# Optimization experiments

Hardware: AMD Instinct MI355X
Metric: run time of the kernel (lower is better)

Reference implementation:

```python
import jax, jax.numpy as jnp
import numpy as np


def setup_inputs() -> dict:
    key = jax.random.key(0)
    ks = jax.random.split(key, 10)
    N, E = 50000, 1600000
    IN, H, OUT = 32, 64, 16
    x = jax.random.normal(ks[0], (N, IN), dtype=jnp.float32)
    edge_index = jax.random.randint(ks[1], (2, E), 0, N, dtype=jnp.int64)
    edge_attr = jax.random.normal(ks[2], (E, 3), dtype=jnp.float32)
    s1 = 1.0 / np.sqrt(2 * IN + 3)
    W1 = jax.random.uniform(ks[3], (2 * IN + 3, H), jnp.float32, -s1, s1)
    b1 = jax.random.uniform(ks[4], (H,), jnp.float32, -s1, s1)
    s2 = 1.0 / np.sqrt(H)
    W2 = jax.random.uniform(ks[5], (H, H), jnp.float32, -s2, s2)
    b2 = jax.random.uniform(ks[6], (H,), jnp.float32, -s2, s2)
    Wo = jax.random.uniform(ks[7], (H, OUT), jnp.float32, -s2, s2)
    bo = jax.random.uniform(ks[8], (OUT,), jnp.float32, -s2, s2)
    return {"x": x, "edge_index": edge_index, "edge_attr": edge_attr,
            "W1": W1, "b1": b1, "W2": W2, "b2": b2, "Wo": Wo, "bo": bo}


def reference(x, edge_index, edge_attr, W1, b1, W2, b2, Wo, bo):
    N = x.shape[0]
    src, dst = edge_index[0], edge_index[1]  # PyG: x_j = x[src], x_i = x[dst]
    x_i = x[dst]                      # [E, IN]
    x_j = x[src]                      # [E, IN]
    tmp = jnp.concatenate([x_i, x_j - x_i, edge_attr], axis=1)  # [E, 2*IN+3]
    h = jax.nn.relu(tmp @ W1 + b1)    # [E, H]
    msg = h @ W2 + b2                 # [E, H]
    # max-aggregate messages to destination nodes; empty segments -> 0 (PyG fill)
    agg = jax.ops.segment_max(msg, dst, num_segments=N)
    agg = jnp.where(jnp.isfinite(agg), agg, 0.0)
    out = jax.nn.sigmoid(agg @ Wo + bo)  # [N, OUT]
    return out
```

## Files before the change

kernel.cpp:

```cpp
#include <hip/hip_runtime.h>

#define IN_F 32
#define HID 64
#define OUTF 16
#define NSUB 8
#define SB_CAP 16
#define OVF_CAP 65536
#define ORD_NEG_INF 0x007FFFFFu

typedef _Float16 v8h __attribute__((ext_vector_type(8)));
typedef float v4f __attribute__((ext_vector_type(4)));

__device__ __forceinline__ unsigned ordenc(float v) {
  unsigned b = __float_as_uint(v);
  return (b & 0x80000000u) ? ~b : (b | 0x80000000u);
}
__device__ __forceinline__ float orddec(unsigned u) {
  unsigned b = (u & 0x80000000u) ? (u & 0x7FFFFFFFu) : ~u;
  return __uint_as_float(b);
}
__device__ __forceinline__ unsigned short f2h_bits(float f) {
  _Float16 h = (_Float16)f; unsigned short u; __builtin_memcpy(&u, &h, 2); return u;
}
__device__ __forceinline__ float h_bits2f(unsigned short u) {
  _Float16 h; __builtin_memcpy(&h, &u, 2); return (float)h;
}

__global__ __launch_bounds__(256) void pre_scatter_kernel(
    const float* __restrict__ x, const int* __restrict__ ei,
    const float* __restrict__ ea, const float* __restrict__ W1,
    const float* __restrict__ b1,
    float* __restrict__ P, float* __restrict__ Q,
    uint2* __restrict__ rec, int* __restrict__ cnt,
    int* __restrict__ ovf, int* __restrict__ ovf_cnt,
    int E, int N, int nSB)
{
  if (blockIdx.x < (unsigned)nSB) {
    const int t = threadIdx.x;
    const int base = blockIdx.x * 1024;
    const int g = blockIdx.x & (NSUB - 1);
    int e[4], s[4], d[4], pos[4];
    bool v[4];
#pragma unroll
    for (int i = 0; i < 4; ++i) {
      e[i] = base + i * 256 + t;
      v[i] = e[i] < E;
      int ec = v[i] ? e[i] : 0;
      s[i] = ei[ec];
      d[i] = ei[(size_t)E + ec];
    }
#pragma unroll
    for (int i = 0; i < 4; ++i)
      pos[i] = v[i] ? atomicAdd(&cnt[d[i] * NSUB + g], 1) : SB_CAP;
    float a0[4], a1[4], a2[4];
#pragma unroll
    for (int i = 0; i < 4; ++i) {
      int ec = v[i] ? e[i] : 0;
      a0[i] = ea[ec * 3 + 0]; a1[i] = ea[ec * 3 + 1]; a2[i] = ea[ec * 3 + 2];
    }
#pragma unroll
    for (int i = 0; i < 4; ++i) {
      if (!v[i]) continue;
      if (pos[i] < SB_CAP) {
        uint2 r;
        r.x = (unsigned)s[i] | ((unsigned)f2h_bits(a0[i]) << 16);
        r.y = (unsigned)f2h_bits(a1[i]) | ((unsigned)f2h_bits(a2[i]) << 16);
        rec[((size_t)d[i] * NSUB + g) * SB_CAP + pos[i]] = r;
      } else {
        int oi = atomicAdd(ovf_cnt, 1);
        if (oi < OVF_CAP) ovf[oi] = e[i];
      }
    }
    return;
  }
  const int lane = threadIdx.x & 63;
  float w1d[IN_F], w1b[IN_F];
#pragma unroll
  for (int c = 0; c < IN_F; ++c) {
    w1b[c] = W1[(IN_F + c) * HID + lane];
    w1d[c] = W1[c * HID + lane] - w1b[c];
  }
  const float b1v = b1[lane];
  int gw = __builtin_amdgcn_readfirstlane((((int)blockIdx.x - nSB) << 2) | (threadIdx.x >> 6));
  const int nwaves = 512 << 2;
  for (int n = gw; n < N; n += nwaves) {
    float p = b1v, q = 0.f;
#pragma unroll
    for (int c = 0; c < IN_F; ++c) {
      float xv = x[n * IN_F + c];
      p = fmaf(xv, w1d[c], p);
      q = fmaf(xv, w1b[c], q);
    }
    P[n * HID + lane] = p;
    Q[n * HID + lane] = q;
  }
}

__global__ __launch_bounds__(256) void bucket_kernel(
    const uint2* __restrict__ rec, const int* __restrict__ cnt,
    const float* __restrict__ W1, const float* __restrict__ W2,
    const float* __restrict__ P, const float* __restrict__ Q,
    unsigned* __restrict__ agg, int N)
{
  __shared__ __align__(16) _Float16 hB[4][16][72];

  const int wave = threadIdx.x >> 6;
  const int lane = threadIdx.x & 63;
  const int quad = lane >> 4;
  const int eidx = lane & 15;
  const int mych = ((eidx >> 2) << 4) + (quad << 2) + (eidx & 3);

  v8h a_frag[4][2];
#pragma unroll
  for (int t = 0; t < 4; ++t)
#pragma unroll
    for (int ks = 0; ks < 2; ++ks)
#pragma unroll
      for (int j = 0; j < 8; ++j)
        a_frag[t][ks][j] = (_Float16)W2[(ks * 32 + quad * 8 + j) * HID + t * 16 + eidx];

  const float w1c0 = W1[(2 * IN_F + 0) * HID + lane];
  const float w1c1 = W1[(2 * IN_F + 1) * HID + lane];
  const float w1c2 = W1[(2 * IN_F + 2) * HID + lane];

  const int gwave = __builtin_amdgcn_readfirstlane((blockIdx.x << 2) | wave);
  const int nw = gridDim.x << 2;

  int d = gwave;
  if (d >= N) return;

  int m; uint2 r0, r1; float pP;
  auto prefetch = [&](int dd) {
    const uint4 ca = *(const uint4*)&cnt[(size_t)dd * NSUB];
    const uint4 cb = *(const uint4*)&cnt[(size_t)dd * NSUB + 4];
    int c0 = min((int)ca.x, SB_CAP), c1 = min((int)ca.y, SB_CAP);
    int c2 = min((int)ca.z, SB_CAP), c3 = min((int)ca.w, SB_CAP);
    int c4 = min((int)cb.x, SB_CAP), c5 = min((int)cb.y, SB_CAP);
    int c6 = min((int)cb.z, SB_CAP), c7 = min((int)cb.w, SB_CAP);
    int p1 = c0, p2 = p1 + c1, p3 = p2 + c2, p4 = p3 + c3;
    int p5 = p4 + c4, p6 = p5 + c5, p7 = p6 + c6;
    m = p7 + c7;
#pragma unroll
    for (int rr = 0; rr < 2; ++rr) {
      int i = rr * 64 + lane;
      if (i < m) {
        int g = 0, base = 0;
        if (i >= p1) { g = 1; base = p1; }
        if (i >= p2) { g = 2; base = p2; }
        if (i >= p3) { g = 3; base = p3; }
        if (i >= p4) { g = 4; base = p4; }
        if (i >= p5) { g = 5; base = p5; }
        if (i >= p6) { g = 6; base = p6; }
        if (i >= p7) { g = 7; base = p7; }
        uint2 rv = rec[((size_t)dd * NSUB + g) * SB_CAP + (i - base)];
        if (rr == 0) r0 = rv; else r1 = rv;
      }
    }
    pP = P[(size_t)dd * HID + lane];
  };

  prefetch(d);

  while (d < N) {
    const int dn = d + nw;
    const int m_cur = m;
    const float pvl = pP;
    uint2 ra = r0, rb = r1;

    if (m_cur > 0) {
      {
        const int lm = m_cur - 1;
        unsigned rlx, rly;
        if (lm < 64) {
          rlx = (unsigned)__builtin_amdgcn_readlane((int)ra.x, lm);
          rly = (unsigned)__builtin_amdgcn_readlane((int)ra.y, lm);
        } else {
          rlx = (unsigned)__builtin_amdgcn_readlane((int)rb.x, lm & 63);
          rly = (unsigned)__builtin_amdgcn_readlane((int)rb.y, lm & 63);
        }
        if (lane >= m_cur)      { ra.x = rlx; ra.y = rly; }
        if (lane + 64 >= m_cur) { rb.x = rlx; rb.y = rly; }
      }

      float qv[16];
#pragma unroll
      for (int i = 0; i < 16; ++i) {
        unsigned sx = (unsigned)__builtin_amdgcn_readlane((int)ra.x, i) & 0xFFFFu;
        qv[i] = Q[(size_t)sx * HID + lane];
      }

      if (dn < N) prefetch(dn);

      float maxv[4][4];
#pragma unroll
      for (int t = 0; t < 4; ++t)
#pragma unroll
        for (int r = 0; r < 4; ++r) maxv[t][r] = -INFINITY;

      const int ntile = (m_cur + 15) >> 4;
      for (int tb = 0; tb < ntile; ++tb) {
        uint2 rs;
        rs.x = (tb < 4) ? ra.x : rb.x;
        rs.y = (tb < 4) ? ra.y : rb.y;
        const int b16 = (tb & 3) << 4;
#pragma unroll
        for (int i = 0; i < 16; ++i) {
          const unsigned rx = (unsigned)__builtin_amdgcn_readlane((int)rs.x, b16 + i);
          const unsigned ry = (unsigned)__builtin_amdgcn_readlane((int)rs.y, b16 + i);
          float pre = pvl + qv[i];
          pre = fmaf(h_bits2f((unsigned short)(rx >> 16)), w1c0, pre);
          pre = fmaf(h_bits2f((unsigned short)(ry & 0xFFFFu)), w1c1, pre);
          pre = fmaf(h_bits2f((unsigned short)(ry >> 16)), w1c2, pre);
          hB[wave][i][lane] = (_Float16)fmaxf(pre, 0.f);
        }
        if (tb + 1 < ntile) {
          const unsigned rnx = (tb + 1 < 4) ? ra.x : rb.x;
          const int b16n = ((tb + 1) & 3) << 4;
#pragma unroll
          for (int i = 0; i < 16; ++i) {
            unsigned sx = (unsigned)__builtin_amdgcn_readlane((int)rnx, b16n + i) & 0xFFFFu;
            qv[i] = Q[(size_t)sx * HID + lane];
          }
        }
        __builtin_amdgcn_wave_barrier();

        const v8h bf0 = *(const v8h*)&hB[wave][eidx][quad * 8];
        const v8h bf1 = *(const v8h*)&hB[wave][eidx][32 + quad * 8];
#pragma unroll
        for (int t = 0; t < 4; ++t) {
          v4f acc = (v4f){0.f, 0.f, 0.f, 0.f};
          acc = __builtin_amdgcn_mfma_f32_16x16x32_f16(a_frag[t][0], bf0, acc, 0, 0, 0);
          acc = __builtin_amdgcn_mfma_f32_16x16x32_f16(a_frag[t][1], bf1, acc, 0, 0, 0);
#pragma unroll
          for (int r = 0; r < 4; ++r) maxv[t][r] = fmaxf(maxv[t][r], acc[r]);
        }
        __builtin_amdgcn_wave_barrier();
      }

#pragma unroll
      for (int t = 0; t < 4; ++t)
#pragma unroll
        for (int r = 0; r < 4; ++r) {
          float v = maxv[t][r];
          v = fmaxf(v, __shfl_xor(v, 1, 64));
          v = fmaxf(v, __shfl_xor(v, 2, 64));
          v = fmaxf(v, __shfl_xor(v, 4, 64));
          v = fmaxf(v, __shfl_xor(v, 8, 64));
          maxv[t][r] = v;
        }
      float val = maxv[0][0];
#pragma unroll
      for (int t = 0; t < 4; ++t)
#pragma unroll
        for (int r = 0; r < 4; ++r)
          val = (eidx == t * 4 + r) ? maxv[t][r] : val;
      agg[(size_t)d * HID + mych] = ordenc(val);
    } else {
      if (dn < N) prefetch(dn);
      agg[(size_t)d * HID + lane] = ORD_NEG_INF;
    }
    d = dn;
  }
}

__global__ __launch_bounds__(256) void overflow_kernel(
    const int* __restrict__ ei, const float* __restrict__ ea,
    const float* __restrict__ W1, const float* __restrict__ W2,
    const float* __restrict__ P, const float* __restrict__ Q,
    const int* __restrict__ ovf, const int* __restrict__ ovf_cnt,
    unsigned* __restrict__ agg, int E)
{
  __shared__ float hsh[4][HID];
  const int wave = threadIdx.x >> 6;
  const int lane = threadIdx.x & 63;

  int M = *ovf_cnt;
  if (M > OVF_CAP) M = OVF_CAP;
  if (M == 0) return;

  float w2r[HID];
#pragma unroll
  for (int j = 0; j < HID; ++j) w2r[j] = W2[j * HID + lane];
  const float w1c0 = W1[(2 * IN_F + 0) * HID + lane];
  const float w1c1 = W1[(2 * IN_F + 1) * HID + lane];
  const float w1c2 = W1[(2 * IN_F + 2) * HID + lane];

  const int gwave = __builtin_amdgcn_readfirstlane((blockIdx.x << 2) | wave);
  const int nw = gridDim.x << 2;
  for (int k = gwave; k < M; k += nw) {
    int e = ovf[k];
    int s = ei[e];
    int d = ei[(size_t)E + e];
    float pre = P[(size_t)d * HID + lane] + Q[(size_t)s * HID + lane];
    pre = fmaf(ea[e * 3 + 0], w1c0, pre);
    pre = fmaf(ea[e * 3 + 1], w1c1, pre);
    pre = fmaf(ea[e * 3 + 2], w1c2, pre);
    hsh[wave][lane] = fmaxf(pre, 0.f);
    __builtin_amdgcn_wave_barrier();
    float mv = 0.f;
#pragma unroll
    for (int j = 0; j < HID; ++j) mv = fmaf(hsh[wave][j], w2r[j], mv);
    atomicMax(&agg[(size_t)d * HID + lane], ordenc(mv));
    __builtin_amdgcn_wave_barrier();
  }
}

__global__ __launch_bounds__(256) void out_kernel(
    const unsigned* __restrict__ agg,
    const float* __restrict__ b2,
    const float* __restrict__ Wo, const float* __restrict__ bo,
    float* __restrict__ out, int N)
{
  __shared__ float Wos[HID * OUTF];
  __shared__ float bos[OUTF];
  __shared__ float b2s[HID];
  __shared__ float aggs[16][HID + 1];

  for (int i = threadIdx.x; i < HID * OUTF; i += 256) Wos[i] = Wo[i];
  if (threadIdx.x < OUTF) bos[threadIdx.x] = bo[threadIdx.x];
  if (threadIdx.x < HID) b2s[threadIdx.x] = b2[threadIdx.x];
  __syncthreads();

  const int nodeBase = blockIdx.x * 16;
  {
    int ln = threadIdx.x >> 4;
    int k0 = (threadIdx.x & 15) * 4;
    int n = nodeBase + ln;
    if (n < N) {
      const uint4 u = *(const uint4*)&agg[n * HID + k0];
      aggs[ln][k0 + 0] = (u.x == ORD_NEG_INF) ? 0.f : orddec(u.x) + b2s[k0 + 0];
      aggs[ln][k0 + 1] = (u.y == ORD_NEG_INF) ? 0.f : orddec(u.y) + b2s[k0 + 1];
      aggs[ln][k0 + 2] = (u.z == ORD_NEG_INF) ? 0.f : orddec(u.z) + b2s[k0 + 2];
      aggs[ln][k0 + 3] = (u.w == ORD_NEG_INF) ? 0.f : orddec(u.w) + b2s[k0 + 3];
    }
  }
  __syncthreads();
  {
    int ln = threadIdx.x >> 4;
    int o = threadIdx.x & 15;
    int n = nodeBase + ln;
    if (n < N) {
      float acc = bos[o];
#pragma unroll
      for (int k = 0; k < HID; ++k) acc = fmaf(aggs[ln][k], Wos[k * OUTF + o], acc);
      out[n * OUTF + o] = 1.f / (1.f + __expf(-acc));
    }
  }
}

extern "C" void kernel_launch(void* const* d_in, const int* in_sizes, int n_in,
                              void* d_out, int out_size, void* d_ws, size_t ws_size,
                              hipStream_t stream) {
  const float* x  = (const float*)d_in[0];
  const int*   ei = (const int*)d_in[1];
  const float* ea = (const float*)d_in[2];
  const float* W1 = (const float*)d_in[3];
  const float* b1 = (const float*)d_in[4];
  const float* W2 = (const float*)d_in[5];
  const float* b2 = (const float*)d_in[6];
  const float* Wo = (const float*)d_in[7];
  const float* bo = (const float*)d_in[8];
  float* out = (float*)d_out;

  const int N = in_sizes[0] / IN_F;
  const int E = in_sizes[1] / 2;

  char* w = (char*)d_ws;
  float*    Pp  = (float*)w;                     w += (size_t)N * HID * 4;
  float*    Qp  = (float*)w;                     w += (size_t)N * HID * 4;
  unsigned* agg = (unsigned*)w;                  w += (size_t)N * HID * 4;
  uint2*    rec = (uint2*)w;                     w += (size_t)N * NSUB * SB_CAP * 8;
  int*      cnt = (int*)w;                       w += (size_t)N * NSUB * 4;
  int*  ovf_cnt = (int*)w;                       w += 16;
  int*      ovf = (int*)w;

  hipMemsetAsync(cnt, 0, (size_t)N * NSUB * 4 + 16, stream);

  const int nSB = (E + 1023) / 1024;
  pre_scatter_kernel<<<nSB + 512, 256, 0, stream>>>(
      x, ei, ea, W1, b1, Pp, Qp, rec, cnt, ovf, ovf_cnt, E, N, nSB);
  bucket_kernel<<<4096, 256, 0, stream>>>(rec, cnt, W1, W2, Pp, Qp, agg, N);
  overflow_kernel<<<256, 256, 0, stream>>>(ei, ea, W1, W2, Pp, Qp, ovf, ovf_cnt, agg, E);
  out_kernel<<<(N + 15) / 16, 256, 0, stream>>>(agg, b2, Wo, bo, out, N);
}
```

Measured before the change: 298.7 us.

## Store Q in fp16 and double-buffer gather loads across MFMA tile pairs

The per-node Q projection is now stored as fp16, halving the bytes of the random gather of Q rows per edge. The edge tile loop is restructured to process two 16-edge tiles per iteration with two register buffers (qvA/qvB), so the gathers for the next tiles are issued before the MFMA work of the current tile, improving latency hiding. This raises register pressure and adds fp16 rounding to Q before the ReLU/max.

Measured after the change: 308.3 us. 1.03x slower.

```diff
diff --git a/kernel.cpp b/kernel.cpp
--- a/kernel.cpp
+++ b/kernel.cpp
@@ -30,7 +30,7 @@
     const float* __restrict__ x, const int* __restrict__ ei,
     const float* __restrict__ ea, const float* __restrict__ W1,
     const float* __restrict__ b1,
-    float* __restrict__ P, float* __restrict__ Q,
+    float* __restrict__ P, _Float16* __restrict__ Q,
     uint2* __restrict__ rec, int* __restrict__ cnt,
     int* __restrict__ ovf, int* __restrict__ ovf_cnt,
     int E, int N, int nSB)
@@ -92,14 +92,14 @@
       q = fmaf(xv, w1b[c], q);
     }
     P[n * HID + lane] = p;
-    Q[n * HID + lane] = q;
+    Q[n * HID + lane] = (_Float16)q;
   }
 }
 
 __global__ __launch_bounds__(256) void bucket_kernel(
     const uint2* __restrict__ rec, const int* __restrict__ cnt,
     const float* __restrict__ W1, const float* __restrict__ W2,
-    const float* __restrict__ P, const float* __restrict__ Q,
+    const float* __restrict__ P, const _Float16* __restrict__ Q,
     unsigned* __restrict__ agg, int N)
 {
   __shared__ __align__(16) _Float16 hB[4][16][72];
@@ -182,11 +182,16 @@
         if (lane + 64 >= m_cur) { rb.x = rlx; rb.y = rly; }
       }
 
-      float qv[16];
+      float qvA[16], qvB[16];
 #pragma unroll
       for (int i = 0; i < 16; ++i) {
         unsigned sx = (unsigned)__builtin_amdgcn_readlane((int)ra.x, i) & 0xFFFFu;
-        qv[i] = Q[(size_t)sx * HID + lane];
+        qvA[i] = (float)Q[(size_t)sx * HID + lane];
+      }
+#pragma unroll
+      for (int i = 0; i < 16; ++i) {
+        unsigned sx = (unsigned)__builtin_amdgcn_readlane((int)ra.x, 16 + i) & 0xFFFFu;
+        qvB[i] = (float)Q[(size_t)sx * HID + lane];
       }
 
       if (dn < N) prefetch(dn);
@@ -198,41 +203,77 @@
         for (int r = 0; r < 4; ++r) maxv[t][r] = -INFINITY;
 
       const int ntile = (m_cur + 15) >> 4;
-      for (int tb = 0; tb < ntile; ++tb) {
-        uint2 rs;
-        rs.x = (tb < 4) ? ra.x : rb.x;
-        rs.y = (tb < 4) ? ra.y : rb.y;
-        const int b16 = (tb & 3) << 4;
+      const int ntp = (ntile + 1) >> 1;
+      for (int tp = 0; tp < ntp; ++tp) {
+        const unsigned rsx = (tp < 2) ? ra.x : rb.x;
+        const unsigned rsy = (tp < 2) ? ra.y : rb.y;
+        const int b0 = (tp & 1) << 5;
+
 #pragma unroll
         for (int i = 0; i < 16; ++i) {
-          const unsigned rx = (unsigned)__builtin_amdgcn_readlane((int)rs.x, b16 + i);
-          const unsigned ry = (unsigned)__builtin_amdgcn_readlane((int)rs.y, b16 + i);
-          float pre = pvl + qv[i];
+          const unsigned rx = (unsigned)__builtin_amdgcn_readlane((int)rsx, b0 + i);
+          const unsigned ry = (unsigned)__builtin_amdgcn_readlane((int)rsy, b0 + i);
+          float pre = pvl + qvA[i];
           pre = fmaf(h_bits2f((unsigned short)(rx >> 16)), w1c0, pre);
           pre = fmaf(h_bits2f((unsigned short)(ry & 0xFFFFu)), w1c1, pre);
           pre = fmaf(h_bits2f((unsigned short)(ry >> 16)), w1c2, pre);
           hB[wave][i][lane] = (_Float16)fmaxf(pre, 0.f);
         }
-        if (tb + 1 < ntile) {
-          const unsigned rnx = (tb + 1 < 4) ? ra.x : rb.x;
-          const int b16n = ((tb + 1) & 3) << 4;
-#pragma unroll
-          for (int i = 0; i < 16; ++i) {
-            unsigned sx = (unsigned)__builtin_amdgcn_readlane((int)rnx, b16n + i) & 0xFFFFu;
-            qv[i] = Q[(size_t)sx * HID + lane];
+        __builtin_amdgcn_wave_barrier();
+        {
+          const v8h bf0 = *(const v8h*)&hB[wave][eidx][quad * 8];
+          const v8h bf1 = *(const v8h*)&hB[wave][eidx][32 + quad * 8];
+          if (tp + 1 < ntp) {
+            const unsigned rnx = (tp + 1 < 2) ? ra.x : rb.x;
+            const int bn = ((tp + 1) & 1) << 5;
+#pragma unroll
+            for (int i = 0; i < 16; ++i) {
+              unsigned sx = (unsigned)__builtin_amdgcn_readlane((int)rnx, bn + i) & 0xFFFFu;
+              qvA[i] = (float)Q[(size_t)sx * HID + lane];
+            }
           }
+#pragma unroll
+          for (int t = 0; t < 4; ++t) {
+            v4f acc = (v4f){0.f, 0.f, 0.f, 0.f};
+            acc = __builtin_amdgcn_mfma_f32_16x16x32_f16(a_frag[t][0], bf0, acc, 0, 0, 0);
+            acc = __builtin_amdgcn_mfma_f32_16x16x32_f16(a_frag[t][1], bf1, acc, 0, 0, 0);
+#pragma unroll
+            for (int r = 0; r < 4; ++r) maxv[t][r] = fmaxf(maxv[t][r], acc[r]);
+          }
         }
         __builtin_amdgcn_wave_barrier();
 
-        const v8h bf0 = *(const v8h*)&hB[wave][eidx][quad * 8];
-        const v8h bf1 = *(const v8h*)&hB[wave][eidx][32 + quad * 8];
-#pragma unroll
-        for (int t = 0; t < 4; ++t) {
-          v4f acc = (v4f){0.f, 0.f, 0.f, 0.f};
-          acc = __builtin_amdgcn_mfma_f32_16x16x32_f16(a_frag[t][0], bf0, acc, 0, 0, 0);
-          acc = __builtin_amdgcn_mfma_f32_16x16x32_f16(a_frag[t][1], bf1, acc, 0, 0, 0);
-#pragma unroll
-          for (int r = 0; r < 4; ++r) maxv[t][r] = fmaxf(maxv[t][r], acc[r]);
+#pragma unroll
+        for (int i = 0; i < 16; ++i) {
+          const unsigned rx = (unsigned)__builtin_amdgcn_readlane((int)rsx, b0 + 16 + i);
+          const unsigned ry = (unsigned)__builtin_amdgcn_readlane((int)rsy, b0 + 16 + i);
+          float pre = pvl + qvB[i];
+          pre = fmaf(h_bits2f((unsigned short)(rx >> 16)), w1c0, pre);
+          pre = fmaf(h_bits2f((unsigned short)(ry & 0xFFFFu)), w1c1, pre);
+          pre = fmaf(h_bits2f((unsigned short)(ry >> 16)), w1c2, pre);
+          hB[wave][i][lane] = (_Float16)fmaxf(pre, 0.f);
+        }
+        __builtin_amdgcn_wave_barrier();
+        {
+          const v8h bf0 = *(const v8h*)&hB[wave][eidx][quad * 8];
+          const v8h bf1 = *(const v8h*)&hB[wave][eidx][32 + quad * 8];
+          if (tp + 1 < ntp) {
+            const unsigned rnx = (tp + 1 < 2) ? ra.x : rb.x;
+            const int bn = ((tp + 1) & 1) << 5;
+#pragma unroll
+            for (int i = 0; i < 16; ++i) {
+              unsigned sx = (unsigned)__builtin_amdgcn_readlane((int)rnx, bn + 16 + i) & 0xFFFFu;
+              qvB[i] = (float)Q[(size_t)sx * HID + lane];
+            }
+          }
+#pragma unroll
+          for (int t = 0; t < 4; ++t) {
+            v4f acc = (v4f){0.f, 0.f, 0.f, 0.f};
+            acc = __builtin_amdgcn_mfma_f32_16x16x32_f16(a_frag[t][0], bf0, acc, 0, 0, 0);
+            acc = __builtin_amdgcn_mfma_f32_16x16x32_f16(a_frag[t][1], bf1, acc, 0, 0, 0);
+#pragma unroll
+            for (int r = 0; r < 4; ++r) maxv[t][r] = fmaxf(maxv[t][r], acc[r]);
+          }
         }
         __builtin_amdgcn_wave_barrier();
       }
@@ -266,7 +307,7 @@
 __global__ __launch_bounds__(256) void overflow_kernel(
     const int* __restrict__ ei, const float* __restrict__ ea,
     const float* __restrict__ W1, const float* __restrict__ W2,
-    const float* __restrict__ P, const float* __restrict__ Q,
+    const float* __restrict__ P, const _Float16* __restrict__ Q,
     const int* __restrict__ ovf, const int* __restrict__ ovf_cnt,
     unsigned* __restrict__ agg, int E)
 {
@@ -291,7 +332,7 @@
     int e = ovf[k];
     int s = ei[e];
     int d = ei[(size_t)E + e];
-    float pre = P[(size_t)d * HID + lane] + Q[(size_t)s * HID + lane];
+    float pre = P[(size_t)d * HID + lane] + (float)Q[(size_t)s * HID + lane];
     pre = fmaf(ea[e * 3 + 0], w1c0, pre);
     pre = fmaf(ea[e * 3 + 1], w1c1, pre);
     pre = fmaf(ea[e * 3 + 2], w1c2, pre);
@@ -366,13 +407,13 @@
   const int E = in_sizes[1] / 2;
 
   char* w = (char*)d_ws;
-  float*    Pp  = (float*)w;                     w += (size_t)N * HID * 4;
-  float*    Qp  = (float*)w;                     w += (size_t)N * HID * 4;
-  unsigned* agg = (unsigned*)w;                  w += (size_t)N * HID * 4;
-  uint2*    rec = (uint2*)w;                     w += (size_t)N * NSUB * SB_CAP * 8;
-  int*      cnt = (int*)w;                       w += (size_t)N * NSUB * 4;
-  int*  ovf_cnt = (int*)w;                       w += 16;
-  int*      ovf = (int*)w;
+  float*     Pp  = (float*)w;                    w += (size_t)N * HID * 4;
+  _Float16*  Qp  = (_Float16*)w;                 w += (size_t)N * HID * 2;
+  unsigned*  agg = (unsigned*)w;                 w += (size_t)N * HID * 4;
+  uint2*     rec = (uint2*)w;                    w += (size_t)N * NSUB * SB_CAP * 8;
+  int*       cnt = (int*)w;                      w += (size_t)N * NSUB * 4;
+  int*   ovf_cnt = (int*)w;                      w += 16;
+  int*       ovf = (int*)w;
 
   hipMemsetAsync(cnt, 0, (size_t)N * NSUB * 4 + 16, stream);
 
```

## Split each destination across two waves, halve sub-buckets, store Q in fp16

Applied to the files above, without the earlier changes.

Each destination node's edge buckets are now split between two waves. Each wave handles two of four sub-buckets, so at most 32 edges fit in a single register. Each wave writes a partial max into one of two agg planes, and the output kernel merges the two planes. Q is stored as fp16 to halve the gather traffic of the per-edge source lookups, and the bucket grid is doubled. This adds agg write and read traffic and fp16 rounding of Q. The smaller bucket capacity may also push more edges to the slower overflow path.

Measured after the change: 335.1 us. 1.12x slower.

```diff
diff --git a/kernel.cpp b/kernel.cpp
--- a/kernel.cpp
+++ b/kernel.cpp
@@ -3,7 +3,7 @@
 #define IN_F 32
 #define HID 64
 #define OUTF 16
-#define NSUB 8
+#define NSUB 4
 #define SB_CAP 16
 #define OVF_CAP 65536
 #define ORD_NEG_INF 0x007FFFFFu
@@ -30,7 +30,7 @@
     const float* __restrict__ x, const int* __restrict__ ei,
     const float* __restrict__ ea, const float* __restrict__ W1,
     const float* __restrict__ b1,
-    float* __restrict__ P, float* __restrict__ Q,
+    float* __restrict__ P, _Float16* __restrict__ Q,
     uint2* __restrict__ rec, int* __restrict__ cnt,
     int* __restrict__ ovf, int* __restrict__ ovf_cnt,
     int E, int N, int nSB)
@@ -92,14 +92,14 @@
       q = fmaf(xv, w1b[c], q);
     }
     P[n * HID + lane] = p;
-    Q[n * HID + lane] = q;
+    Q[n * HID + lane] = (_Float16)q;
   }
 }
 
 __global__ __launch_bounds__(256) void bucket_kernel(
     const uint2* __restrict__ rec, const int* __restrict__ cnt,
     const float* __restrict__ W1, const float* __restrict__ W2,
-    const float* __restrict__ P, const float* __restrict__ Q,
+    const float* __restrict__ P, const _Float16* __restrict__ Q,
     unsigned* __restrict__ agg, int N)
 {
   __shared__ __align__(16) _Float16 hB[4][16][72];
@@ -125,71 +125,51 @@
 
   const int gwave = __builtin_amdgcn_readfirstlane((blockIdx.x << 2) | wave);
   const int nw = gridDim.x << 2;
-
-  int d = gwave;
-  if (d >= N) return;
-
-  int m; uint2 r0, r1; float pP;
-  auto prefetch = [&](int dd) {
-    const uint4 ca = *(const uint4*)&cnt[(size_t)dd * NSUB];
-    const uint4 cb = *(const uint4*)&cnt[(size_t)dd * NSUB + 4];
-    int c0 = min((int)ca.x, SB_CAP), c1 = min((int)ca.y, SB_CAP);
-    int c2 = min((int)ca.z, SB_CAP), c3 = min((int)ca.w, SB_CAP);
-    int c4 = min((int)cb.x, SB_CAP), c5 = min((int)cb.y, SB_CAP);
-    int c6 = min((int)cb.z, SB_CAP), c7 = min((int)cb.w, SB_CAP);
-    int p1 = c0, p2 = p1 + c1, p3 = p2 + c2, p4 = p3 + c3;
-    int p5 = p4 + c4, p6 = p5 + c5, p7 = p6 + c6;
-    m = p7 + c7;
-#pragma unroll
-    for (int rr = 0; rr < 2; ++rr) {
-      int i = rr * 64 + lane;
-      if (i < m) {
-        int g = 0, base = 0;
-        if (i >= p1) { g = 1; base = p1; }
-        if (i >= p2) { g = 2; base = p2; }
-        if (i >= p3) { g = 3; base = p3; }
-        if (i >= p4) { g = 4; base = p4; }
-        if (i >= p5) { g = 5; base = p5; }
-        if (i >= p6) { g = 6; base = p6; }
-        if (i >= p7) { g = 7; base = p7; }
-        uint2 rv = rec[((size_t)dd * NSUB + g) * SB_CAP + (i - base)];
-        if (rr == 0) r0 = rv; else r1 = rv;
-      }
+  const int NI = 2 * N;
+
+  int w = gwave;
+  if (w >= NI) return;
+
+  int m; uint2 r0; float pP;
+  auto prefetch = [&](int ww) {
+    const int dd = ww >> 1, hh = ww & 1;
+    const uint2 cc = *(const uint2*)&cnt[(size_t)dd * NSUB + 2 * hh];
+    const int c0 = min((int)cc.x, SB_CAP), c1 = min((int)cc.y, SB_CAP);
+    m = c0 + c1;
+    if (lane < m) {
+      const int gg = (lane < c0) ? 2 * hh : 2 * hh + 1;
+      const int off = (lane < c0) ? lane : lane - c0;
+      r0 = rec[((size_t)dd * NSUB + gg) * SB_CAP + off];
     }
     pP = P[(size_t)dd * HID + lane];
   };
 
-  prefetch(d);
-
-  while (d < N) {
-    const int dn = d + nw;
+  prefetch(w);
+
+  while (w < NI) {
+    const int wn = w + nw;
     const int m_cur = m;
     const float pvl = pP;
-    uint2 ra = r0, rb = r1;
+    uint2 ra = r0;
+    const int d = w >> 1, h = w & 1;
+    unsigned* aggrow = agg + ((size_t)h * N + (size_t)d) * HID;
 
     if (m_cur > 0) {
       {
         const int lm = m_cur - 1;
-        unsigned rlx, rly;
-        if (lm < 64) {
-          rlx = (unsigned)__builtin_amdgcn_readlane((int)ra.x, lm);
-          rly = (unsigned)__builtin_amdgcn_readlane((int)ra.y, lm);
-        } else {
-          rlx = (unsigned)__builtin_amdgcn_readlane((int)rb.x, lm & 63);
-          rly = (unsigned)__builtin_amdgcn_readlane((int)rb.y, lm & 63);
-        }
-        if (lane >= m_cur)      { ra.x = rlx; ra.y = rly; }
-        if (lane + 64 >= m_cur) { rb.x = rlx; rb.y = rly; }
+        const unsigned rlx = (unsigned)__builtin_amdgcn_readlane((int)ra.x, lm);
+        const unsigned rly = (unsigned)__builtin_amdgcn_readlane((int)ra.y, lm);
+        if (lane >= m_cur) { ra.x = rlx; ra.y = rly; }
       }
 
       float qv[16];
 #pragma unroll
       for (int i = 0; i < 16; ++i) {
         unsigned sx = (unsigned)__builtin_amdgcn_readlane((int)ra.x, i) & 0xFFFFu;
-        qv[i] = Q[(size_t)sx * HID + lane];
+        qv[i] = (float)Q[(size_t)sx * HID + lane];
       }
 
-      if (dn < N) prefetch(dn);
+      if (wn < NI) prefetch(wn);
 
       float maxv[4][4];
 #pragma unroll
@@ -199,33 +179,28 @@
 
       const int ntile = (m_cur + 15) >> 4;
       for (int tb = 0; tb < ntile; ++tb) {
-        uint2 rs;
-        rs.x = (tb < 4) ? ra.x : rb.x;
-        rs.y = (tb < 4) ? ra.y : rb.y;
-        const int b16 = (tb & 3) << 4;
+        const int b16 = tb << 4;
 #pragma unroll
         for (int i = 0; i < 16; ++i) {
-          const unsigned rx = (unsigned)__builtin_amdgcn_readlane((int)rs.x, b16 + i);
-          const unsigned ry = (unsigned)__builtin_amdgcn_readlane((int)rs.y, b16 + i);
+          const unsigned rx = (unsigned)__builtin_amdgcn_readlane((int)ra.x, b16 + i);
+          const unsigned ry = (unsigned)__builtin_amdgcn_readlane((int)ra.y, b16 + i);
           float pre = pvl + qv[i];
           pre = fmaf(h_bits2f((unsigned short)(rx >> 16)), w1c0, pre);
           pre = fmaf(h_bits2f((unsigned short)(ry & 0xFFFFu)), w1c1, pre);
           pre = fmaf(h_bits2f((unsigned short)(ry >> 16)), w1c2, pre);
           hB[wave][i][lane] = (_Float16)fmaxf(pre, 0.f);
         }
+        __builtin_amdgcn_wave_barrier();
+
+        const v8h bf0 = *(const v8h*)&hB[wave][eidx][quad * 8];
+        const v8h bf1 = *(const v8h*)&hB[wave][eidx][32 + quad * 8];
         if (tb + 1 < ntile) {
-          const unsigned rnx = (tb + 1 < 4) ? ra.x : rb.x;
-          const int b16n = ((tb + 1) & 3) << 4;
 #pragma unroll
           for (int i = 0; i < 16; ++i) {
-            unsigned sx = (unsigned)__builtin_amdgcn_readlane((int)rnx, b16n + i) & 0xFFFFu;
-            qv[i] = Q[(size_t)sx * HID + lane];
+            unsigned sx = (unsigned)__builtin_amdgcn_readlane((int)ra.x, 16 + i) & 0xFFFFu;
+            qv[i] = (float)Q[(size_t)sx * HID + lane];
           }
         }
-        __builtin_amdgcn_wave_barrier();
-
-        const v8h bf0 = *(const v8h*)&hB[wave][eidx][quad * 8];
-        const v8h bf1 = *(const v8h*)&hB[wave][eidx][32 + quad * 8];
 #pragma unroll
         for (int t = 0; t < 4; ++t) {
           v4f acc = (v4f){0.f, 0.f, 0.f, 0.f};
@@ -254,19 +229,19 @@
 #pragma unroll
         for (int r = 0; r < 4; ++r)
           val = (eidx == t * 4 + r) ? maxv[t][r] : val;
-      agg[(size_t)d * HID + mych] = ordenc(val);
+      aggrow[mych] = ordenc(val);
     } else {
-      if (dn < N) prefetch(dn);
-      agg[(size_t)d * HID + lane] = ORD_NEG_INF;
-    }
-    d = dn;
+      if (wn < NI) prefetch(wn);
+      aggrow[lane] = ORD_NEG_INF;
+    }
+    w = wn;
   }
 }
 
 __global__ __launch_bounds__(256) void overflow_kernel(
     const int* __restrict__ ei, const float* __restrict__ ea,
     const float* __restrict__ W1, const float* __restrict__ W2,
-    const float* __restrict__ P, const float* __restrict__ Q,
+    const float* __restrict__ P, const _Float16* __restrict__ Q,
     const int* __restrict__ ovf, const int* __restrict__ ovf_cnt,
     unsigned* __restrict__ agg, int E)
 {
@@ -291,7 +266,7 @@
     int e = ovf[k];
     int s = ei[e];
     int d = ei[(size_t)E + e];
-    float pre = P[(size_t)d * HID + lane] + Q[(size_t)s * HID + lane];
+    float pre = P[(size_t)d * HID + lane] + (float)Q[(size_t)s * HID + lane];
     pre = fmaf(ea[e * 3 + 0], w1c0, pre);
     pre = fmaf(ea[e * 3 + 1], w1c1, pre);
     pre = fmaf(ea[e * 3 + 2], w1c2, pre);
@@ -327,11 +302,14 @@
     int k0 = (threadIdx.x & 15) * 4;
     int n = nodeBase + ln;
     if (n < N) {
-      const uint4 u = *(const uint4*)&agg[n * HID + k0];
-      aggs[ln][k0 + 0] = (u.x == ORD_NEG_INF) ? 0.f : orddec(u.x) + b2s[k0 + 0];
-      aggs[ln][k0 + 1] = (u.y == ORD_NEG_INF) ? 0.f : orddec(u.y) + b2s[k0 + 1];
-      aggs[ln][k0 + 2] = (u.z == ORD_NEG_INF) ? 0.f : orddec(u.z) + b2s[k0 + 2];
-      aggs[ln][k0 + 3] = (u.w == ORD_NEG_INF) ? 0.f : orddec(u.w) + b2s[k0 + 3];
+      const uint4 uA = *(const uint4*)&agg[((size_t)n) * HID + k0];
+      const uint4 uB = *(const uint4*)&agg[((size_t)N + n) * HID + k0];
+      const unsigned m0 = max(uA.x, uB.x), m1 = max(uA.y, uB.y);
+      const unsigned m2 = max(uA.z, uB.z), m3 = max(uA.w, uB.w);
+      aggs[ln][k0 + 0] = (m0 == ORD_NEG_INF) ? 0.f : orddec(m0) + b2s[k0 + 0];
+      aggs[ln][k0 + 1] = (m1 == ORD_NEG_INF) ? 0.f : orddec(m1) + b2s[k0 + 1];
+      aggs[ln][k0 + 2] = (m2 == ORD_NEG_INF) ? 0.f : orddec(m2) + b2s[k0 + 2];
+      aggs[ln][k0 + 3] = (m3 == ORD_NEG_INF) ? 0.f : orddec(m3) + b2s[k0 + 3];
     }
   }
   __syncthreads();
@@ -366,20 +344,20 @@
   const int E = in_sizes[1] / 2;
 
   char* w = (char*)d_ws;
-  float*    Pp  = (float*)w;                     w += (size_t)N * HID * 4;
-  float*    Qp  = (float*)w;                     w += (size_t)N * HID * 4;
-  unsigned* agg = (unsigned*)w;                  w += (size_t)N * HID * 4;
-  uint2*    rec = (uint2*)w;                     w += (size_t)N * NSUB * SB_CAP * 8;
-  int*      cnt = (int*)w;                       w += (size_t)N * NSUB * 4;
-  int*  ovf_cnt = (int*)w;                       w += 16;
-  int*      ovf = (int*)w;
+  float*     Pp  = (float*)w;                    w += (size_t)N * HID * 4;
+  _Float16*  Qp  = (_Float16*)w;                 w += (size_t)N * HID * 2;
+  unsigned*  agg = (unsigned*)w;                 w += (size_t)2 * N * HID * 4;
+  uint2*     rec = (uint2*)w;                    w += (size_t)N * NSUB * SB_CAP * 8;
+  int*       cnt = (int*)w;                      w += (size_t)N * NSUB * 4;
+  int*   ovf_cnt = (int*)w;                      w += 16;
+  int*       ovf = (int*)w;
 
   hipMemsetAsync(cnt, 0, (size_t)N * NSUB * 4 + 16, stream);
 
   const int nSB = (E + 1023) / 1024;
   pre_scatter_kernel<<<nSB + 512, 256, 0, stream>>>(
       x, ei, ea, W1, b1, Pp, Qp, rec, cnt, ovf, ovf_cnt, E, N, nSB);
-  bucket_kernel<<<4096, 256, 0, stream>>>(rec, cnt, W1, W2, Pp, Qp, agg, N);
+  bucket_kernel<<<8192, 256, 0, stream>>>(rec, cnt, W1, W2, Pp, Qp, agg, N);
   overflow_kernel<<<256, 256, 0, stream>>>(ei, ea, W1, W2, Pp, Qp, ovf, ovf_cnt, agg, E);
   out_kernel<<<(N + 15) / 16, 256, 0, stream>>>(agg, b2, Wo, bo, out, N);
 }
```

## Switch bucket MFMA to 32x32x16 tiles and store Q projection in fp16

Applied to the files above, without the earlier changes.

The bucket kernel now processes 32 edges per tile with 32x32x16 f16 MFMAs instead of 16-edge tiles with 16x16x32 MFMAs. This halves the tile count and changes the accumulator layout, output channel mapping and reduction shuffles to match. Separately, the per-node Q projection is stored as fp16, halving the bytes fetched in the random source-node gathers. The fp16 Q adds rounding error, and the larger tiles raise register pressure (32 qv values plus 32 max accumulators) and waste work on nodes with few edges.

Measured after the change: 394.0 us. 31.9% more time.

```diff
diff --git a/kernel.cpp b/kernel.cpp
--- a/kernel.cpp
+++ b/kernel.cpp
@@ -9,7 +9,7 @@
 #define ORD_NEG_INF 0x007FFFFFu
 
 typedef _Float16 v8h __attribute__((ext_vector_type(8)));
-typedef float v4f __attribute__((ext_vector_type(4)));
+typedef float v16f __attribute__((ext_vector_type(16)));
 
 __device__ __forceinline__ unsigned ordenc(float v) {
   unsigned b = __float_as_uint(v);
@@ -30,7 +30,7 @@
     const float* __restrict__ x, const int* __restrict__ ei,
     const float* __restrict__ ea, const float* __restrict__ W1,
     const float* __restrict__ b1,
-    float* __restrict__ P, float* __restrict__ Q,
+    float* __restrict__ P, _Float16* __restrict__ Q,
     uint2* __restrict__ rec, int* __restrict__ cnt,
     int* __restrict__ ovf, int* __restrict__ ovf_cnt,
     int E, int N, int nSB)
@@ -92,32 +92,32 @@
       q = fmaf(xv, w1b[c], q);
     }
     P[n * HID + lane] = p;
-    Q[n * HID + lane] = q;
+    Q[n * HID + lane] = (_Float16)q;
   }
 }
 
 __global__ __launch_bounds__(256) void bucket_kernel(
     const uint2* __restrict__ rec, const int* __restrict__ cnt,
     const float* __restrict__ W1, const float* __restrict__ W2,
-    const float* __restrict__ P, const float* __restrict__ Q,
+    const float* __restrict__ P, const _Float16* __restrict__ Q,
     unsigned* __restrict__ agg, int N)
 {
-  __shared__ __align__(16) _Float16 hB[4][16][72];
+  __shared__ __align__(16) _Float16 hB[4][32][72];
 
   const int wave = threadIdx.x >> 6;
   const int lane = threadIdx.x & 63;
-  const int quad = lane >> 4;
-  const int eidx = lane & 15;
-  const int mych = ((eidx >> 2) << 4) + (quad << 2) + (eidx & 3);
-
-  v8h a_frag[4][2];
-#pragma unroll
-  for (int t = 0; t < 4; ++t)
-#pragma unroll
-    for (int ks = 0; ks < 2; ++ks)
+  const int lo5 = lane & 31;
+  const int hi = lane >> 5;
+  const int mych = (lane & 3) | ((lane >> 5) << 2) | (((lane >> 2) & 3) << 3) | (((lane >> 4) & 1) << 5);
+
+  v8h a_frag[2][4];
+#pragma unroll
+  for (int t = 0; t < 2; ++t)
+#pragma unroll
+    for (int ks = 0; ks < 4; ++ks)
 #pragma unroll
       for (int j = 0; j < 8; ++j)
-        a_frag[t][ks][j] = (_Float16)W2[(ks * 32 + quad * 8 + j) * HID + t * 16 + eidx];
+        a_frag[t][ks][j] = (_Float16)W2[(ks * 16 + hi * 8 + j) * HID + t * 32 + lo5];
 
   const float w1c0 = W1[(2 * IN_F + 0) * HID + lane];
   const float w1c1 = W1[(2 * IN_F + 1) * HID + lane];
@@ -182,78 +182,84 @@
         if (lane + 64 >= m_cur) { rb.x = rlx; rb.y = rly; }
       }
 
-      float qv[16];
-#pragma unroll
-      for (int i = 0; i < 16; ++i) {
+      float qv[32];
+#pragma unroll
+      for (int i = 0; i < 32; ++i) {
         unsigned sx = (unsigned)__builtin_amdgcn_readlane((int)ra.x, i) & 0xFFFFu;
-        qv[i] = Q[(size_t)sx * HID + lane];
+        qv[i] = (float)Q[(size_t)sx * HID + lane];
       }
 
       if (dn < N) prefetch(dn);
 
-      float maxv[4][4];
-#pragma unroll
-      for (int t = 0; t < 4; ++t)
-#pragma unroll
-        for (int r = 0; r < 4; ++r) maxv[t][r] = -INFINITY;
-
-      const int ntile = (m_cur + 15) >> 4;
+      float maxv[2][16];
+#pragma unroll
+      for (int t = 0; t < 2; ++t)
+#pragma unroll
+        for (int r = 0; r < 16; ++r) maxv[t][r] = -INFINITY;
+
+      const int ntile = (m_cur + 31) >> 5;
       for (int tb = 0; tb < ntile; ++tb) {
-        uint2 rs;
-        rs.x = (tb < 4) ? ra.x : rb.x;
-        rs.y = (tb < 4) ? ra.y : rb.y;
-        const int b16 = (tb & 3) << 4;
-#pragma unroll
-        for (int i = 0; i < 16; ++i) {
-          const unsigned rx = (unsigned)__builtin_amdgcn_readlane((int)rs.x, b16 + i);
-          const unsigned ry = (unsigned)__builtin_amdgcn_readlane((int)rs.y, b16 + i);
+        const unsigned rsx = (tb < 2) ? ra.x : rb.x;
+        const unsigned rsy = (tb < 2) ? ra.y : rb.y;
+        const int b0 = (tb & 1) << 5;
+#pragma unroll
+        for (int i = 0; i < 32; ++i) {
+          const unsigned rx = (unsigned)__builtin_amdgcn_readlane((int)rsx, b0 + i);
+          const unsigned ry = (unsigned)__builtin_amdgcn_readlane((int)rsy, b0 + i);
           float pre = pvl + qv[i];
           pre = fmaf(h_bits2f((unsigned short)(rx >> 16)), w1c0, pre);
           pre = fmaf(h_bits2f((unsigned short)(ry & 0xFFFFu)), w1c1, pre);
           pre = fmaf(h_bits2f((unsigned short)(ry >> 16)), w1c2, pre);
           hB[wave][i][lane] = (_Float16)fmaxf(pre, 0.f);
         }
+        __builtin_amdgcn_wave_barrier();
+
+        const v8h bf0 = *(const v8h*)&hB[wave][lo5][0 + hi * 8];
+        const v8h bf1 = *(const v8h*)&hB[wave][lo5][16 + hi * 8];
+        const v8h bf2 = *(const v8h*)&hB[wave][lo5][32 + hi * 8];
+        const v8h bf3 = *(const v8h*)&hB[wave][lo5][48 + hi * 8];
+
         if (tb + 1 < ntile) {
-          const unsigned rnx = (tb + 1 < 4) ? ra.x : rb.x;
-          const int b16n = ((tb + 1) & 3) << 4;
-#pragma unroll
-          for (int i = 0; i < 16; ++i) {
-            unsigned sx = (unsigned)__builtin_amdgcn_readlane((int)rnx, b16n + i) & 0xFFFFu;
-            qv[i] = Q[(size_t)sx * HID + lane];
+          const unsigned rnx = (tb + 1 < 2) ? ra.x : rb.x;
+          const int bn = ((tb + 1) & 1) << 5;
+#pragma unroll
+          for (int i = 0; i < 32; ++i) {
+            unsigned sx = (unsigned)__builtin_amdgcn_readlane((int)rnx, bn + i) & 0xFFFFu;
+            qv[i] = (float)Q[(size_t)sx * HID + lane];
           }
         }
+
+#pragma unroll
+        for (int t = 0; t < 2; ++t) {
+          v16f acc = (v16f)(0.f);
+          acc = __builtin_amdgcn_mfma_f32_32x32x16_f16(a_frag[t][0], bf0, acc, 0, 0, 0);
+          acc = __builtin_amdgcn_mfma_f32_32x32x16_f16(a_frag[t][1], bf1, acc, 0, 0, 0);
+          acc = __builtin_amdgcn_mfma_f32_32x32x16_f16(a_frag[t][2], bf2, acc, 0, 0, 0);
+          acc = __builtin_amdgcn_mfma_f32_32x32x16_f16(a_frag[t][3], bf3, acc, 0, 0, 0);
+#pragma unroll
+          for (int r = 0; r < 16; ++r) maxv[t][r] = fmaxf(maxv[t][r], acc[r]);
+        }
         __builtin_amdgcn_wave_barrier();
-
-        const v8h bf0 = *(const v8h*)&hB[wave][eidx][quad * 8];
-        const v8h bf1 = *(const v8h*)&hB[wave][eidx][32 + quad * 8];
-#pragma unroll
-        for (int t = 0; t < 4; ++t) {
-          v4f acc = (v4f){0.f, 0.f, 0.f, 0.f};
-          acc = __builtin_amdgcn_mfma_f32_16x16x32_f16(a_frag[t][0], bf0, acc, 0, 0, 0);
-          acc = __builtin_amdgcn_mfma_f32_16x16x32_f16(a_frag[t][1], bf1, acc, 0, 0, 0);
-#pragma unroll
-          for (int r = 0; r < 4; ++r) maxv[t][r] = fmaxf(maxv[t][r], acc[r]);
-        }
-        __builtin_amdgcn_wave_barrier();
-      }
-
-#pragma unroll
-      for (int t = 0; t < 4; ++t)
-#pragma unroll
-        for (int r = 0; r < 4; ++r) {
+      }
+
+#pragma unroll
+      for (int t = 0; t < 2; ++t)
+#pragma unroll
+        for (int r = 0; r < 16; ++r) {
           float v = maxv[t][r];
           v = fmaxf(v, __shfl_xor(v, 1, 64));
           v = fmaxf(v, __shfl_xor(v, 2, 64));
           v = fmaxf(v, __shfl_xor(v, 4, 64));
           v = fmaxf(v, __shfl_xor(v, 8, 64));
+          v = fmaxf(v, __shfl_xor(v, 16, 64));
           maxv[t][r] = v;
         }
       float val = maxv[0][0];
 #pragma unroll
-      for (int t = 0; t < 4; ++t)
-#pragma unroll
-        for (int r = 0; r < 4; ++r)
-          val = (eidx == t * 4 + r) ? maxv[t][r] : val;
+      for (int t = 0; t < 2; ++t)
+#pragma unroll
+        for (int r = 0; r < 16; ++r)
+          val = ((((lane >> 4) & 1) == t) && ((lane & 15) == r)) ? maxv[t][r] : val;
       agg[(size_t)d * HID + mych] = ordenc(val);
     } else {
       if (dn < N) prefetch(dn);
@@ -266,7 +272,7 @@
 __global__ __launch_bounds__(256) void overflow_kernel(
     const int* __restrict__ ei, const float* __restrict__ ea,
     const float* __restrict__ W1, const float* __restrict__ W2,
-    const float* __restrict__ P, const float* __restrict__ Q,
+    const float* __restrict__ P, const _Float16* __restrict__ Q,
     const int* __restrict__ ovf, const int* __restrict__ ovf_cnt,
     unsigned* __restrict__ agg, int E)
 {
@@ -291,7 +297,7 @@
     int e = ovf[k];
     int s = ei[e];
     int d = ei[(size_t)E + e];
-    float pre = P[(size_t)d * HID + lane] + Q[(size_t)s * HID + lane];
+    float pre = P[(size_t)d * HID + lane] + (float)Q[(size_t)s * HID + lane];
     pre = fmaf(ea[e * 3 + 0], w1c0, pre);
     pre = fmaf(ea[e * 3 + 1], w1c1, pre);
     pre = fmaf(ea[e * 3 + 2], w1c2, pre);
@@ -327,7 +333,7 @@
     int k0 = (threadIdx.x & 15) * 4;
     int n = nodeBase + ln;
     if (n < N) {
-      const uint4 u = *(const uint4*)&agg[n * HID + k0];
+      const uint4 u = *(const uint4*)&agg[(size_t)n * HID + k0];
       aggs[ln][k0 + 0] = (u.x == ORD_NEG_INF) ? 0.f : orddec(u.x) + b2s[k0 + 0];
       aggs[ln][k0 + 1] = (u.y == ORD_NEG_INF) ? 0.f : orddec(u.y) + b2s[k0 + 1];
       aggs[ln][k0 + 2] = (u.z == ORD_NEG_INF) ? 0.f : orddec(u.z) + b2s[k0 + 2];
@@ -366,13 +372,13 @@
   const int E = in_sizes[1] / 2;
 
   char* w = (char*)d_ws;
-  float*    Pp  = (float*)w;                     w += (size_t)N * HID * 4;
-  float*    Qp  = (float*)w;                     w += (size_t)N * HID * 4;
-  unsigned* agg = (unsigned*)w;                  w += (size_t)N * HID * 4;
-  uint2*    rec = (uint2*)w;                     w += (size_t)N * NSUB * SB_CAP * 8;
-  int*      cnt = (int*)w;                       w += (size_t)N * NSUB * 4;
-  int*  ovf_cnt = (int*)w;                       w += 16;
-  int*      ovf = (int*)w;
+  float*     Pp  = (float*)w;                    w += (size_t)N * HID * 4;
+  _Float16*  Qp  = (_Float16*)w;                 w += (size_t)N * HID * 2;
+  unsigned*  agg = (unsigned*)w;                 w += (size_t)N * HID * 4;
+  uint2*     rec = (uint2*)w;                    w += (size_t)N * NSUB * SB_CAP * 8;
+  int*       cnt = (int*)w;                      w += (size_t)N * NSUB * 4;
+  int*   ovf_cnt = (int*)w;                      w += 16;
+  int*       ovf = (int*)w;
 
   hipMemsetAsync(cnt, 0, (size_t)N * NSUB * 4 + 16, stream);
 
```
